# Kernel tuning notes

Measured on AMD Instinct MI355X. Metric: run time of the kernel, lower is better.

Reference implementation:

```python
import jax, jax.numpy as jnp
import numpy as np

EPS = 0.05  # blend weight of K_Rectify smoothing


def k_rectify(x_nbc, distance, idx, eps=EPS):
    """Distance-weighted neighbor smoothing.
    x_nbc: (N, B, C); distance, idx: (B, N, K). Returns (N, B, C)."""
    x_bnc = jnp.transpose(x_nbc, (1, 0, 2))                       # (B,N,C)
    B = x_bnc.shape[0]
    neigh = x_bnc[jnp.arange(B)[:, None, None], idx]              # (B,N,K,C) gather
    w = jax.nn.softmax(-distance, axis=-1)                        # closer -> larger weight
    smoothed = jnp.einsum('bnk,bnkc->bnc', w, neigh)              # (B,N,C)
    y = (1.0 - eps) * x_bnc + eps * smoothed
    return jnp.transpose(y, (1, 0, 2))


def monarch_linear(x, w1, w2, bias):
    """Monarch block-diagonal butterfly multiply on the last dim.
    w1: (k,q,p), w2: (l,s,r) with k*p == n, l*r == k*q."""
    shp = x.shape
    k, q, p = w1.shape
    l, s, r = w2.shape
    xb = x.reshape(-1, k, p)
    o1 = jnp.einsum('kqp,bkp->bkq', w1, xb)                       # (B*, k, q)
    o1 = o1.reshape(-1, r, l).transpose(0, 2, 1)                  # 'b (r l) -> b l r'
    o2 = jnp.einsum('lsr,blr->bls', w2, o1)                       # (B*, l, s)
    out = o2.transpose(0, 2, 1).reshape(-1, s * l) + bias         # 'b l s -> b (s l)'
    return out.reshape(*shp[:-1], s * l)


def setup_inputs() -> dict:
    key = jax.random.key(0)
    B, N, C, K, nblocks = 8, 8192, 256, 8, 8
    blk = C // nblocks
    ks = jax.random.split(key, 6)
    x = jax.random.normal(ks[0], (B, N, C), dtype=jnp.float32)
    distance = jax.random.uniform(ks[1], (B, N, K), dtype=jnp.float32)
    idx = jax.random.randint(ks[2], (B, N, K), 0, N)
    rf = jax.random.normal(ks[3], (B, N, C), dtype=jnp.float32)
    scale = 1.0 / np.sqrt(blk)
    w1 = jax.random.normal(ks[4], (nblocks, blk, blk), dtype=jnp.float32) * scale
    w2 = jax.random.normal(ks[5], (nblocks, blk, blk), dtype=jnp.float32) * scale
    bias = jnp.zeros((C,), dtype=jnp.float32)
    return {"x": x, "distance": distance, "idx": idx, "rf": rf,
            "w1": w1, "w2": w2, "bias": bias}


def reference(x, distance, idx, rf, w1, w2, bias):
    # _prepare_in: (B,N,C) -> (N,B,C)
    xs = jnp.transpose(x, (1, 0, 2))
    s1 = k_rectify(xs, distance, idx)            # smooth_in
    t = monarch_linear(s1, w1, w2, bias)         # Monarch block-diag matmul
    s2 = k_rectify(t, distance, idx)             # smooth_out
    return jnp.transpose(s2, (1, 0, 2)) + rf     # _out_transform residual
```

## Files before the change

kernel.cpp:

```cpp
#include <hip/hip_runtime.h>

#define NPTS 8192
#define CH   256
#define KNB  8
#define NROWS 65536
#define ROWS_PER_BLK 16
#define ROWS_PER_IT  4

typedef unsigned short ushort_t;

__device__ __forceinline__ ushort_t f32_to_bf16(float f) {
    unsigned int b = __float_as_uint(f);
    b += 0x7FFFu + ((b >> 16) & 1u);
    return (ushort_t)(b >> 16);
}
__device__ __forceinline__ float bf16_to_f32(ushort_t u) {
    return __uint_as_float(((unsigned int)u) << 16);
}

__global__ __launch_bounds__(256) void pm_stage1(
    const float* __restrict__ x, const float* __restrict__ dist,
    const int* __restrict__ idx, const float* __restrict__ w1,
    const float* __restrict__ w2, const float* __restrict__ bias,
    ushort_t* __restrict__ t)
{
    const int c = threadIdx.x;

    __shared__ float s1[ROWS_PER_IT][CH];
    __shared__ float fmid[ROWS_PER_IT][CH];

    float4 w1r[8], w2r[8];
    {
        const float4* w1p = (const float4*)(w1 + c * 32);
        const float4* w2p = (const float4*)(w2 + ((c & 7) * 32 + (c >> 3)) * 32);
#pragma unroll
        for (int i = 0; i < 8; ++i) { w1r[i] = w1p[i]; w2r[i] = w2p[i]; }
    }
    const float bb = bias[c];
    const int l2 = c & 7;
    const int kb = c >> 5;

    const int rr   = __builtin_amdgcn_readfirstlane(threadIdx.x >> 6);
    const int lane = threadIdx.x & 63;

    const int row_base = blockIdx.x * ROWS_PER_BLK;
    const int b = row_base >> 13;
    const float4* x4 = (const float4*)(x + (size_t)b * NPTS * CH);

    for (int it = 0; it < ROWS_PER_BLK / ROWS_PER_IT; ++it) {
        const int row  = row_base + it * ROWS_PER_IT + rr;
        const int rloc = row & (NPTS - 1);

        float d[KNB]; int nb[KNB];
#pragma unroll
        for (int k = 0; k < KNB; ++k) {
            d[k]  = dist[(size_t)row * KNB + k];
            nb[k] = idx[(size_t)row * KNB + k];
        }
        float mn = d[0];
#pragma unroll
        for (int k = 1; k < KNB; ++k) mn = fminf(mn, d[k]);
        float e[KNB]; float sum = 0.f;
#pragma unroll
        for (int k = 0; k < KNB; ++k) { e[k] = __expf(mn - d[k]); sum += e[k]; }
        const float inv = 0.05f / sum;

        float4 acc = x4[(size_t)rloc * 64 + lane];
        acc.x *= 0.95f; acc.y *= 0.95f; acc.z *= 0.95f; acc.w *= 0.95f;
#pragma unroll
        for (int k = 0; k < KNB; ++k) {
            const float4 g = x4[(size_t)nb[k] * 64 + lane];
            const float w = e[k] * inv;
            acc.x += w * g.x; acc.y += w * g.y; acc.z += w * g.z; acc.w += w * g.w;
        }
        ((float4*)&s1[rr][0])[lane] = acc;
        __syncthreads();

#pragma unroll
        for (int r2 = 0; r2 < ROWS_PER_IT; ++r2) {
            const float4* sb = (const float4*)(&s1[r2][kb * 32]);
            float a = 0.f;
#pragma unroll
            for (int p4 = 0; p4 < 8; ++p4) {
                const float4 s = sb[p4];
                a += w1r[p4].x * s.x + w1r[p4].y * s.y
                   + w1r[p4].z * s.z + w1r[p4].w * s.w;
            }
            fmid[r2][c] = a;
        }
        __syncthreads();

#pragma unroll
        for (int r2 = 0; r2 < ROWS_PER_IT; ++r2) {
            float a = bb;
#pragma unroll
            for (int r4 = 0; r4 < 8; ++r4) {
                a += w2r[r4].x * fmid[r2][(4 * r4 + 0) * 8 + l2];
                a += w2r[r4].y * fmid[r2][(4 * r4 + 1) * 8 + l2];
                a += w2r[r4].z * fmid[r2][(4 * r4 + 2) * 8 + l2];
                a += w2r[r4].w * fmid[r2][(4 * r4 + 3) * 8 + l2];
            }
            t[(size_t)(row_base + it * ROWS_PER_IT + r2) * CH + c] = f32_to_bf16(a);
        }
        __syncthreads();
    }
}

__global__ __launch_bounds__(256) void pm_stage2(
    const ushort_t* __restrict__ t, const float* __restrict__ dist,
    const int* __restrict__ idx, const float* __restrict__ rf,
    float* __restrict__ out)
{
    const int w    = __builtin_amdgcn_readfirstlane(threadIdx.x >> 6);
    const int lane = threadIdx.x & 63;
    const int wrow0 = blockIdx.x * 16 + w * 4;
    const int b     = wrow0 >> 13;
    const ushort4* tb = (const ushort4*)(t + (size_t)b * NPTS * CH);

#pragma unroll
    for (int r = 0; r < 4; ++r) {
        const int row  = wrow0 + r;
        const int rloc = row & (NPTS - 1);

        float d[KNB]; int nb[KNB];
#pragma unroll
        for (int k = 0; k < KNB; ++k) {
            d[k]  = dist[(size_t)row * KNB + k];
            nb[k] = idx[(size_t)row * KNB + k];
        }
        float mn = d[0];
#pragma unroll
        for (int k = 1; k < KNB; ++k) mn = fminf(mn, d[k]);
        float e[KNB]; float sum = 0.f;
#pragma unroll
        for (int k = 0; k < KNB; ++k) { e[k] = __expf(mn - d[k]); sum += e[k]; }
        const float inv = 0.05f / sum;

        const ushort4 c0 = tb[(size_t)rloc * 64 + lane];
        ushort4 g[KNB];
#pragma unroll
        for (int k = 0; k < KNB; ++k) g[k] = tb[(size_t)nb[k] * 64 + lane];

        float4 acc;
        acc.x = 0.95f * bf16_to_f32(c0.x);
        acc.y = 0.95f * bf16_to_f32(c0.y);
        acc.z = 0.95f * bf16_to_f32(c0.z);
        acc.w = 0.95f * bf16_to_f32(c0.w);
#pragma unroll
        for (int k = 0; k < KNB; ++k) {
            const float wk = e[k] * inv;
            acc.x += wk * bf16_to_f32(g[k].x);
            acc.y += wk * bf16_to_f32(g[k].y);
            acc.z += wk * bf16_to_f32(g[k].z);
            acc.w += wk * bf16_to_f32(g[k].w);
        }

        const float4 rv = ((const float4*)rf)[(size_t)row * 64 + lane];
        acc.x += rv.x; acc.y += rv.y; acc.z += rv.z; acc.w += rv.w;
        ((float4*)out)[(size_t)row * 64 + lane] = acc;
    }
}

extern "C" void kernel_launch(void* const* d_in, const int* in_sizes, int n_in,
                              void* d_out, int out_size, void* d_ws, size_t ws_size,
                              hipStream_t stream) {
    const float* x    = (const float*)d_in[0];
    const float* dist = (const float*)d_in[1];
    const int*   idx  = (const int*)d_in[2];
    const float* rf   = (const float*)d_in[3];
    const float* w1   = (const float*)d_in[4];
    const float* w2   = (const float*)d_in[5];
    const float* bias = (const float*)d_in[6];
    float* out = (float*)d_out;
    ushort_t* t = (ushort_t*)d_ws;

    pm_stage1<<<NROWS / ROWS_PER_BLK, 256, 0, stream>>>(x, dist, idx, w1, w2, bias, t);
    pm_stage2<<<NROWS / 16, 256, 0, stream>>>(t, dist, idx, rf, out);
}
```

Baseline: 281.1 us.

## Pre-convert input to bf16, transpose Monarch mid buffer, batch stage2 gathers

After: 279.3 us. No clear change (-0.6%).

```diff
diff --git a/kernel.cpp b/kernel.cpp
--- a/kernel.cpp
+++ b/kernel.cpp
@@ -6,6 +6,7 @@
 #define NROWS 65536
 #define ROWS_PER_BLK 16
 #define ROWS_PER_IT  4
+#define FT_STRIDE 36
 
 typedef unsigned short ushort_t;
 
@@ -17,9 +18,26 @@
 __device__ __forceinline__ float bf16_to_f32(ushort_t u) {
     return __uint_as_float(((unsigned int)u) << 16);
 }
+__device__ __forceinline__ unsigned int pack_bf16(float lo, float hi) {
+    return (unsigned int)f32_to_bf16(lo) | ((unsigned int)f32_to_bf16(hi) << 16);
+}
+
+__global__ __launch_bounds__(256) void pm_conv(
+    const float4* __restrict__ x, uint4* __restrict__ xb)
+{
+    const size_t i = (size_t)blockIdx.x * 256 + threadIdx.x;
+    const float4 a = x[2 * i];
+    const float4 c = x[2 * i + 1];
+    uint4 o;
+    o.x = pack_bf16(a.x, a.y);
+    o.y = pack_bf16(a.z, a.w);
+    o.z = pack_bf16(c.x, c.y);
+    o.w = pack_bf16(c.z, c.w);
+    xb[i] = o;
+}
 
 __global__ __launch_bounds__(256) void pm_stage1(
-    const float* __restrict__ x, const float* __restrict__ dist,
+    const ushort_t* __restrict__ xb, const float* __restrict__ dist,
     const int* __restrict__ idx, const float* __restrict__ w1,
     const float* __restrict__ w2, const float* __restrict__ bias,
     ushort_t* __restrict__ t)
@@ -27,7 +45,7 @@
     const int c = threadIdx.x;
 
     __shared__ float s1[ROWS_PER_IT][CH];
-    __shared__ float fmid[ROWS_PER_IT][CH];
+    __shared__ float fT[ROWS_PER_IT][8 * FT_STRIDE];
 
     float4 w1r[8], w2r[8];
     {
@@ -37,15 +55,16 @@
         for (int i = 0; i < 8; ++i) { w1r[i] = w1p[i]; w2r[i] = w2p[i]; }
     }
     const float bb = bias[c];
-    const int l2 = c & 7;
-    const int kb = c >> 5;
+    const int l2   = c & 7;
+    const int kb   = c >> 5;
+    const int ftw  = l2 * FT_STRIDE + (c >> 3);
 
     const int rr   = __builtin_amdgcn_readfirstlane(threadIdx.x >> 6);
     const int lane = threadIdx.x & 63;
 
     const int row_base = blockIdx.x * ROWS_PER_BLK;
     const int b = row_base >> 13;
-    const float4* x4 = (const float4*)(x + (size_t)b * NPTS * CH);
+    const ushort4* x4 = (const ushort4*)(xb + (size_t)b * NPTS * CH);
 
     for (int it = 0; it < ROWS_PER_BLK / ROWS_PER_IT; ++it) {
         const int row  = row_base + it * ROWS_PER_IT + rr;
@@ -57,6 +76,12 @@
             d[k]  = dist[(size_t)row * KNB + k];
             nb[k] = idx[(size_t)row * KNB + k];
         }
+
+        const ushort4 c0 = x4[(size_t)rloc * 64 + lane];
+        ushort4 g[KNB];
+#pragma unroll
+        for (int k = 0; k < KNB; ++k) g[k] = x4[(size_t)nb[k] * 64 + lane];
+
         float mn = d[0];
 #pragma unroll
         for (int k = 1; k < KNB; ++k) mn = fminf(mn, d[k]);
@@ -65,13 +90,18 @@
         for (int k = 0; k < KNB; ++k) { e[k] = __expf(mn - d[k]); sum += e[k]; }
         const float inv = 0.05f / sum;
 
-        float4 acc = x4[(size_t)rloc * 64 + lane];
-        acc.x *= 0.95f; acc.y *= 0.95f; acc.z *= 0.95f; acc.w *= 0.95f;
-#pragma unroll
-        for (int k = 0; k < KNB; ++k) {
-            const float4 g = x4[(size_t)nb[k] * 64 + lane];
+        float4 acc;
+        acc.x = 0.95f * bf16_to_f32(c0.x);
+        acc.y = 0.95f * bf16_to_f32(c0.y);
+        acc.z = 0.95f * bf16_to_f32(c0.z);
+        acc.w = 0.95f * bf16_to_f32(c0.w);
+#pragma unroll
+        for (int k = 0; k < KNB; ++k) {
             const float w = e[k] * inv;
-            acc.x += w * g.x; acc.y += w * g.y; acc.z += w * g.z; acc.w += w * g.w;
+            acc.x += w * bf16_to_f32(g[k].x);
+            acc.y += w * bf16_to_f32(g[k].y);
+            acc.z += w * bf16_to_f32(g[k].z);
+            acc.w += w * bf16_to_f32(g[k].w);
         }
         ((float4*)&s1[rr][0])[lane] = acc;
         __syncthreads();
@@ -86,19 +116,19 @@
                 a += w1r[p4].x * s.x + w1r[p4].y * s.y
                    + w1r[p4].z * s.z + w1r[p4].w * s.w;
             }
-            fmid[r2][c] = a;
+            fT[r2][ftw] = a;
         }
         __syncthreads();
 
 #pragma unroll
         for (int r2 = 0; r2 < ROWS_PER_IT; ++r2) {
+            const float4* fp = (const float4*)(&fT[r2][l2 * FT_STRIDE]);
             float a = bb;
 #pragma unroll
             for (int r4 = 0; r4 < 8; ++r4) {
-                a += w2r[r4].x * fmid[r2][(4 * r4 + 0) * 8 + l2];
-                a += w2r[r4].y * fmid[r2][(4 * r4 + 1) * 8 + l2];
-                a += w2r[r4].z * fmid[r2][(4 * r4 + 2) * 8 + l2];
-                a += w2r[r4].w * fmid[r2][(4 * r4 + 3) * 8 + l2];
+                const float4 f = fp[r4];
+                a += w2r[r4].x * f.x + w2r[r4].y * f.y
+                   + w2r[r4].z * f.z + w2r[r4].w * f.w;
             }
             t[(size_t)(row_base + it * ROWS_PER_IT + r2) * CH + c] = f32_to_bf16(a);
         }
@@ -111,53 +141,57 @@
     const int* __restrict__ idx, const float* __restrict__ rf,
     float* __restrict__ out)
 {
-    const int w    = __builtin_amdgcn_readfirstlane(threadIdx.x >> 6);
-    const int lane = threadIdx.x & 63;
+    const int w     = __builtin_amdgcn_readfirstlane(threadIdx.x >> 6);
+    const int lane  = threadIdx.x & 63;
     const int wrow0 = blockIdx.x * 16 + w * 4;
     const int b     = wrow0 >> 13;
     const ushort4* tb = (const ushort4*)(t + (size_t)b * NPTS * CH);
 
+    int   nb[4][KNB];
+    float d [4][KNB];
+#pragma unroll
+    for (int r = 0; r < 4; ++r)
+#pragma unroll
+        for (int k = 0; k < KNB; ++k) {
+            nb[r][k] = idx[(size_t)(wrow0 + r) * KNB + k];
+            d [r][k] = dist[(size_t)(wrow0 + r) * KNB + k];
+        }
+
+    ushort4 c0[4], g[4][KNB];
+    float4  rv[4];
 #pragma unroll
     for (int r = 0; r < 4; ++r) {
-        const int row  = wrow0 + r;
-        const int rloc = row & (NPTS - 1);
-
-        float d[KNB]; int nb[KNB];
-#pragma unroll
-        for (int k = 0; k < KNB; ++k) {
-            d[k]  = dist[(size_t)row * KNB + k];
-            nb[k] = idx[(size_t)row * KNB + k];
-        }
-        float mn = d[0];
-#pragma unroll
-        for (int k = 1; k < KNB; ++k) mn = fminf(mn, d[k]);
+        const int rloc = (wrow0 + r) & (NPTS - 1);
+        c0[r] = tb[(size_t)rloc * 64 + lane];
+        rv[r] = ((const float4*)rf)[(size_t)(wrow0 + r) * 64 + lane];
+#pragma unroll
+        for (int k = 0; k < KNB; ++k) g[r][k] = tb[(size_t)nb[r][k] * 64 + lane];
+    }
+
+#pragma unroll
+    for (int r = 0; r < 4; ++r) {
+        float mn = d[r][0];
+#pragma unroll
+        for (int k = 1; k < KNB; ++k) mn = fminf(mn, d[r][k]);
         float e[KNB]; float sum = 0.f;
 #pragma unroll
-        for (int k = 0; k < KNB; ++k) { e[k] = __expf(mn - d[k]); sum += e[k]; }
+        for (int k = 0; k < KNB; ++k) { e[k] = __expf(mn - d[r][k]); sum += e[k]; }
         const float inv = 0.05f / sum;
 
-        const ushort4 c0 = tb[(size_t)rloc * 64 + lane];
-        ushort4 g[KNB];
-#pragma unroll
-        for (int k = 0; k < KNB; ++k) g[k] = tb[(size_t)nb[k] * 64 + lane];
-
         float4 acc;
-        acc.x = 0.95f * bf16_to_f32(c0.x);
-        acc.y = 0.95f * bf16_to_f32(c0.y);
-        acc.z = 0.95f * bf16_to_f32(c0.z);
-        acc.w = 0.95f * bf16_to_f32(c0.w);
+        acc.x = 0.95f * bf16_to_f32(c0[r].x) + rv[r].x;
+        acc.y = 0.95f * bf16_to_f32(c0[r].y) + rv[r].y;
+        acc.z = 0.95f * bf16_to_f32(c0[r].z) + rv[r].z;
+        acc.w = 0.95f * bf16_to_f32(c0[r].w) + rv[r].w;
 #pragma unroll
         for (int k = 0; k < KNB; ++k) {
             const float wk = e[k] * inv;
-            acc.x += wk * bf16_to_f32(g[k].x);
-            acc.y += wk * bf16_to_f32(g[k].y);
-            acc.z += wk * bf16_to_f32(g[k].z);
-            acc.w += wk * bf16_to_f32(g[k].w);
-        }
-
-        const float4 rv = ((const float4*)rf)[(size_t)row * 64 + lane];
-        acc.x += rv.x; acc.y += rv.y; acc.z += rv.z; acc.w += rv.w;
-        ((float4*)out)[(size_t)row * 64 + lane] = acc;
+            acc.x += wk * bf16_to_f32(g[r][k].x);
+            acc.y += wk * bf16_to_f32(g[r][k].y);
+            acc.z += wk * bf16_to_f32(g[r][k].z);
+            acc.w += wk * bf16_to_f32(g[r][k].w);
+        }
+        ((float4*)out)[(size_t)(wrow0 + r) * 64 + lane] = acc;
     }
 }
 
@@ -172,8 +206,11 @@
     const float* w2   = (const float*)d_in[5];
     const float* bias = (const float*)d_in[6];
     float* out = (float*)d_out;
-    ushort_t* t = (ushort_t*)d_ws;
-
-    pm_stage1<<<NROWS / ROWS_PER_BLK, 256, 0, stream>>>(x, dist, idx, w1, w2, bias, t);
+
+    ushort_t* t  = (ushort_t*)d_ws;
+    ushort_t* xb = (ushort_t*)((char*)d_ws + (size_t)NROWS * CH * 2);
+
+    pm_conv  <<<NROWS * CH / (256 * 8), 256, 0, stream>>>((const float4*)x, (uint4*)xb);
+    pm_stage1<<<NROWS / ROWS_PER_BLK, 256, 0, stream>>>(xb, dist, idx, w1, w2, bias, t);
     pm_stage2<<<NROWS / 16, 256, 0, stream>>>(t, dist, idx, rf, out);
 }
```
